# Optimization experiments

Hardware: AMD Instinct MI355X
Metric: run time of the kernel (lower is better)

The kernel has to match this reference:

```python
import jax, jax.numpy as jnp
import numpy as np

N_NODES = 2048
N_FLUID = 400000
N_SOLID = 400000


def setup_inputs() -> dict:
    key = jax.random.key(0)
    k1, k2, k3 = jax.random.split(key, 3)
    nodes = jax.random.uniform(k1, (N_NODES, 3), dtype=jnp.float32)
    # sorted distinct node ids per tet: sort 4 draws from [0, N-4) then add offsets 0..3
    fe = jnp.sort(jax.random.randint(k2, (N_FLUID, 4), 0, N_NODES - 4), axis=1) + jnp.arange(4)
    se = jnp.sort(jax.random.randint(k3, (N_SOLID, 4), 0, N_NODES - 4), axis=1) + jnp.arange(4)
    return {
        "nodes": nodes,
        "fluid_elements": fe.astype(jnp.int32),
        "solid_elements": se.astype(jnp.int32),
        "E_mod": jnp.float32(2.1e11),
        "nu": jnp.float32(0.3),
        "rho_s": jnp.float32(7850.0),
    }


def _grads_and_volume(coords):
    """coords: [E,4,3] -> shape-fn gradients [E,4,3], volume [E]."""
    ones = jnp.ones(coords.shape[:-1] + (1,), coords.dtype)
    A = jnp.concatenate([ones, coords], axis=-1)
    A_inv = jnp.linalg.inv(A)
    grads = jnp.swapaxes(A_inv[..., 1:, :], -1, -2)        # [E,4,3]
    v0 = coords[:, 1] - coords[:, 0]
    v1 = coords[:, 2] - coords[:, 0]
    v2 = coords[:, 3] - coords[:, 0]
    vol = jnp.abs(jnp.linalg.det(jnp.stack([v0, v1, v2], axis=-1))) / 6.0  # [E]
    return grads, vol


def _fluid_element_matrices(coords):
    grads, vol = _grads_and_volume(coords)
    K_e = vol[:, None, None] * jnp.einsum("eik,ejk->eij", grads, grads)      # [E,4,4]
    m_template = (2.0 * jnp.eye(4, dtype=coords.dtype) + jnp.ones((4, 4), coords.dtype)) / 10.0
    M_e = vol[:, None, None] * m_template
    return K_e, M_e


def _elasticity_D(E_mod, nu):
    coeff = E_mod / ((1.0 + nu) * (1.0 - 2.0 * nu))
    top = nu * jnp.ones((3, 3), jnp.float32) + (1.0 - 2.0 * nu) * jnp.eye(3, dtype=jnp.float32)
    D = jnp.zeros((6, 6), jnp.float32)
    D = D.at[:3, :3].set(top)
    D = D.at[3:, 3:].set(((1.0 - 2.0 * nu) / 2.0) * jnp.eye(3, dtype=jnp.float32))
    return coeff * D


def _solid_element_matrices(coords, E_mod, nu, rho_s):
    grads, vol = _grads_and_volume(coords)                 # grads [E,4,3]
    bx, by, bz = grads[..., 0], grads[..., 1], grads[..., 2]   # each [E,4]
    z = jnp.zeros_like(bx)
    # per-node 6x3 strain-displacement block -> [E,4,6,3]
    block = jnp.stack([
        jnp.stack([bx, z, z], axis=-1),
        jnp.stack([z, by, z], axis=-1),
        jnp.stack([z, z, bz], axis=-1),
        jnp.stack([by, bx, z], axis=-1),
        jnp.stack([z, bz, by], axis=-1),
        jnp.stack([bz, z, bx], axis=-1),
    ], axis=-2)
    E = coords.shape[0]
    B = jnp.transpose(block, (0, 2, 1, 3)).reshape(E, 6, 12)  # [E,6,12]
    D = _elasticity_D(E_mod, nu)                              # [6,6]
    K_e = vol[:, None, None] * jnp.einsum("eai,ab,ebj->eij", B, D, B)  # [E,12,12]
    M_e = (rho_s * vol / 4.0)[:, None, None] * jnp.eye(12, dtype=coords.dtype)
    return K_e, M_e


def reference(nodes, fluid_elements, solid_elements, E_mod, nu, rho_s):
    n = nodes.shape[0]
    # ---- fluid: local matrices + scatter-add assembly into [N,N] ----
    cf = nodes[fluid_elements]                              # [Ef,4,3]
    Kf_e, Mf_e = _fluid_element_matrices(cf)
    rows = fluid_elements[:, :, None]                       # [Ef,4,1]
    cols = fluid_elements[:, None, :]                       # [Ef,1,4]
    K_f = jnp.zeros((n, n), jnp.float32).at[rows, cols].add(Kf_e)
    M_f = jnp.zeros((n, n), jnp.float32).at[rows, cols].add(Mf_e)
    # ---- solid: 3 dof/node, assembly into [3N,3N] ----
    cs = nodes[solid_elements]                              # [Es,4,3]
    Ks_e, Ms_e = _solid_element_matrices(cs, E_mod, nu, rho_s)
    dofs = (3 * solid_elements[:, :, None] + jnp.arange(3)).reshape(solid_elements.shape[0], 12)
    K_s = jnp.zeros((3 * n, 3 * n), jnp.float32).at[dofs[:, :, None], dofs[:, None, :]].add(Ks_e)
    M_s = jnp.zeros((3 * n, 3 * n), jnp.float32).at[dofs[:, :, None], dofs[:, None, :]].add(Ms_e)
    return (K_f, M_f, K_s, M_s)
```

## Files before the change

### kernel.cpp

```cpp
#include <hip/hip_runtime.h>


#define G_PART 256
#define BT 512
#define GW (BT / 64)
#define TCAP 1024
#define NCPT 4
#define VSTRIDE 13

__device__ __forceinline__ float sel4(float x0, float x1, float x2, float x3, int a) {
    float r = x0;
    r = (a == 1) ? x1 : r;
    r = (a == 2) ? x2 : r;
    r = (a == 3) ? x3 : r;
    return r;
}
__device__ __forceinline__ int sel4i(int x0, int x1, int x2, int x3, int a) {
    int r = x0;
    r = (a == 1) ? x1 : r;
    r = (a == 2) ? x2 : r;
    r = (a == 3) ? x3 : r;
    return r;
}

__device__ __forceinline__ float wave_reduce(float v) {
#pragma unroll
    for (int m = 1; m < 64; m <<= 1) v += __shfl_xor(v, m, 64);
    return v;
}

__device__ __forceinline__ void tet_geom_f(const float* __restrict__ nodes,
                                           int n0, int n1, int n2, int n3_,
                                           float& gx1, float& gy1, float& gz1,
                                           float& gx2, float& gy2, float& gz2,
                                           float& gx3, float& gy3, float& gz3,
                                           float& volf)
{
    const float* q0 = nodes + 3ll * n0;
    const float* q1 = nodes + 3ll * n1;
    const float* q2 = nodes + 3ll * n2;
    const float* q3 = nodes + 3ll * n3_;
    double p0x = q0[0], p0y = q0[1], p0z = q0[2];
    double r1x = (double)q1[0] - p0x, r1y = (double)q1[1] - p0y, r1z = (double)q1[2] - p0z;
    double r2x = (double)q2[0] - p0x, r2y = (double)q2[1] - p0y, r2z = (double)q2[2] - p0z;
    double r3x = (double)q3[0] - p0x, r3y = (double)q3[1] - p0y, r3z = (double)q3[2] - p0z;
    double c23x = r2y*r3z - r2z*r3y, c23y = r2z*r3x - r2x*r3z, c23z = r2x*r3y - r2y*r3x;
    double det = r1x*c23x + r1y*c23y + r1z*c23z;
    double inv = 1.0 / det;
    double c31x = r3y*r1z - r3z*r1y, c31y = r3z*r1x - r3x*r1z, c31z = r3x*r1y - r3y*r1x;
    double c12x = r1y*r2z - r1z*r2y, c12y = r1z*r2x - r1x*r2z, c12z = r1x*r2y - r1y*r2x;
    gx1 = (float)(c23x*inv); gy1 = (float)(c23y*inv); gz1 = (float)(c23z*inv);
    gx2 = (float)(c31x*inv); gy2 = (float)(c31y*inv); gz2 = (float)(c31z*inv);
    gx3 = (float)(c12x*inv); gy3 = (float)(c12y*inv); gz3 = (float)(c12z*inv);
    volf = (float)(fabs(det) / 6.0);
}

__device__ __forceinline__ int fetch_entry_bs(const int* __restrict__ ent,
                                              const int* __restrict__ Sb,
                                              const int* __restrict__ Qb,
                                              int chunk4, int v)
{
    int lo = 0, hi = 255;
#pragma unroll
    for (int it = 0; it < 8; ++it) {
        int mid = (lo + hi + 1) >> 1;
        bool ge = (Qb[mid] <= v);
        lo = ge ? mid : lo;
        hi = ge ? hi : mid - 1;
    }
    return ent[(size_t)lo * chunk4 + Sb[lo] + (v - Qb[lo])];
}

__global__ void __launch_bounds__(256)
index_build(const int4* __restrict__ fe, const int4* __restrict__ se,
            int* __restrict__ entF, int* __restrict__ entS,
            int* __restrict__ PF, int* __restrict__ PS,
            int nf, int ns, int n, int chunkF, int chunkS)
{
    extern __shared__ int h[];
    int* wsum = h + n;
    const bool solid = blockIdx.x >= G_PART;
    const int b = solid ? blockIdx.x - G_PART : blockIdx.x;
    const int4* elems = solid ? se : fe;
    const int nelem = solid ? ns : nf;
    const int chunk = solid ? chunkS : chunkF;
    int* P2 = solid ? PS : PF;
    int* entries = (solid ? entS : entF) + (size_t)b * 4 * chunk;

    const int t = threadIdx.x;
    const int beg = b * chunk, end = min(nelem, beg + chunk);

    for (int i = t; i < n; i += 256) h[i] = 0;
    __syncthreads();
    for (int e = beg + t; e < end; e += 256) {
        int4 nd = elems[e];
        atomicAdd(&h[nd.x], 1);
        atomicAdd(&h[nd.y], 1);
        atomicAdd(&h[nd.z], 1);
        atomicAdd(&h[nd.w], 1);
    }
    __syncthreads();

    const int cs = (n + 255) / 256;
    const int base = t * cs;
    int s = 0;
    for (int k = 0; k < cs; ++k) {
        int i = base + k;
        if (i < n) s += h[i];
    }
    wsum[t] = s;
    __syncthreads();
    for (int d = 1; d < 256; d <<= 1) {
        int v = (t >= d) ? wsum[t - d] : 0;
        __syncthreads();
        wsum[t] += v;
        __syncthreads();
    }
    int run = (t == 0) ? 0 : wsum[t - 1];
    for (int k = 0; k < cs; ++k) {
        int i = base + k;
        if (i < n) {
            int c = h[i]; h[i] = run;
            P2[(size_t)i * G_PART + b] = run;
            run += c;
        }
    }
    if (t == 255) P2[(size_t)n * G_PART + b] = wsum[255];
    __syncthreads();

    for (int e = beg + t; e < end; e += 256) {
        int4 nd = elems[e];
        int p;
        p = atomicAdd(&h[nd.x], 1); entries[p] = e * 4 + 0;
        p = atomicAdd(&h[nd.y], 1); entries[p] = e * 4 + 1;
        p = atomicAdd(&h[nd.z], 1); entries[p] = e * 4 + 2;
        p = atomicAdd(&h[nd.w], 1); entries[p] = e * 4 + 3;
    }
}

__global__ void __launch_bounds__(BT, 2)
fused_gather(const int* __restrict__ entF, const int* __restrict__ PF,
             const int* __restrict__ entS, const int* __restrict__ PS,
             const int4* __restrict__ fe, const int4* __restrict__ se,
             const float* __restrict__ nodes,
             float* __restrict__ Kf, float* __restrict__ Mf,
             float* __restrict__ Ks, float* __restrict__ Ms,
             const float* __restrict__ E_p, const float* __restrict__ nu_p,
             const float* __restrict__ rho_p, int n, int n3,
             int chunk4F, int chunk4S)
{
    extern __shared__ unsigned char smem[];
    float* vis  = (float*)smem;
    int*   pcnt = (int*)(vis + TCAP * VSTRIDE);
    int*   plist = pcnt + n;
    int*   Sb   = plist + 3 * TCAP;
    int*   Qb   = Sb + 256;
    int*   wsp  = Qb + 257;
    float* dred = (float*)(wsp + GW);

    const int tid = threadIdx.x;
    const int bid = blockIdx.x;
    const bool isSolid = bid < n;
    const int r = isSolid ? bid : bid - n;
    const int* ent = isSolid ? entS : entF;
    const int* P2  = isSolid ? PS : PF;
    const int4* elems4 = isSolid ? se : fe;
    const int chunk4 = isSolid ? chunk4S : chunk4F;

    if (tid < 256) {
        int s0 = P2[(size_t)r * G_PART + tid];
        int e0 = P2[(size_t)(r + 1) * G_PART + tid];
        Sb[tid] = s0;
        Qb[tid] = e0 - s0;
    }
    __syncthreads();
    if (tid < 64) {
        int c0 = Qb[4*tid], c1 = Qb[4*tid+1], c2 = Qb[4*tid+2], c3 = Qb[4*tid+3];
        int s = c0 + c1 + c2 + c3;
        int x = s;
#pragma unroll
        for (int d = 1; d < 64; d <<= 1) {
            int y = __shfl_up(x, d, 64);
            if (tid >= d) x += y;
        }
        int ex = x - s;
        Qb[4*tid] = ex; Qb[4*tid+1] = ex + c0;
        Qb[4*tid+2] = ex + c0 + c1; Qb[4*tid+3] = ex + c0 + c1 + c2;
        if (tid == 63) Qb[256] = ex + s;
    }
    __syncthreads();
    const int T = Qb[256];

    const float E = *E_p, nu = *nu_p, rho = *rho_p;
    const float coeff = E / ((1.f + nu) * (1.f - 2.f * nu));
    const float lam = coeff * nu;
    const float mu  = coeff * (1.f - 2.f * nu) * 0.5f;

    if (isSolid) {
        float acc[NCPT][9];
#pragma unroll
        for (int k = 0; k < NCPT; ++k)
#pragma unroll
            for (int j = 0; j < 9; ++j) acc[k][j] = 0.f;
        float d00=0,d01=0,d02=0,d10=0,d11=0,d12=0,d20=0,d21=0,d22=0,vsum=0;

        for (int vb = 0; vb < T; vb += TCAP) {
            const int Tb = min(T - vb, TCAP);
            for (int c = tid; c < n; c += BT) pcnt[c] = 0;
            __syncthreads();

            for (int v = tid; v < Tb; v += BT) {
                int pk = fetch_entry_bs(ent, Sb, Qb, chunk4, vb + v);
                int e_ = pk >> 2, a = pk & 3;
                int4 nd = elems4[e_];
                float g1x,g1y,g1z,g2x,g2y,g2z,g3x,g3y,g3z,vol;
                tet_geom_f(nodes, nd.x, nd.y, nd.z, nd.w,
                           g1x,g1y,g1z, g2x,g2y,g2z, g3x,g3y,g3z, vol);
                float g0x = -(g1x+g2x+g3x), g0y = -(g1y+g2y+g3y), g0z = -(g1z+g2z+g3z);
                float* V = vis + v * VSTRIDE;
                V[0]=g1x; V[1]=g1y; V[2]=g1z; V[3]=g2x; V[4]=g2y; V[5]=g2z;
                V[6]=g3x; V[7]=g3y; V[8]=g3z; V[9]=vol;
                ((int*)V)[10] = nd.x | (nd.y << 11) | (a << 22);
                ((int*)V)[11] = nd.z | (nd.w << 11);
                float ga0 = sel4(g0x,g1x,g2x,g3x,a);
                float ga1 = sel4(g0y,g1y,g2y,g3y,a);
                float ga2 = sel4(g0z,g1z,g2z,g3z,a);
                {
                    float lv = lam*vol, mv = mu*vol, lm = lv+mv;
                    float mgg = mv*(ga0*ga0 + ga1*ga1 + ga2*ga2);
                    d00 += lm*ga0*ga0 + mgg; d01 += lm*ga0*ga1;       d02 += lm*ga0*ga2;
                    d10 += lm*ga1*ga0;       d11 += lm*ga1*ga1 + mgg; d12 += lm*ga1*ga2;
                    d20 += lm*ga2*ga0;       d21 += lm*ga2*ga1;       d22 += lm*ga2*ga2 + mgg;
                    vsum += vol;
                }
#pragma unroll
                for (int s = 0; s < 3; ++s) {
                    int b = s + ((s >= a) ? 1 : 0);
                    int cb = sel4i(nd.x, nd.y, nd.z, nd.w, b);
                    atomicAdd(&pcnt[cb], 1);
                }
            }
            __syncthreads();

            {
                const int cs = (n + BT - 1) / BT;
                int cb0 = tid * cs;
                int s = 0;
                for (int k = 0; k < cs; ++k) {
                    int i = cb0 + k;
                    if (i < n) s += pcnt[i];
                }
                int x = s;
#pragma unroll
                for (int d = 1; d < 64; d <<= 1) {
                    int y = __shfl_up(x, d, 64);
                    if ((tid & 63) >= d) x += y;
                }
                if ((tid & 63) == 63) wsp[tid >> 6] = x;
                __syncthreads();
                if (tid == 0) {
                    int run = 0;
                    for (int w = 0; w < GW; ++w) { int t_ = wsp[w]; wsp[w] = run; run += t_; }
                }
                __syncthreads();
                int ex = (x - s) + wsp[tid >> 6];
                for (int k = 0; k < cs; ++k) {
                    int i = cb0 + k;
                    if (i < n) { int c0 = pcnt[i]; pcnt[i] = ex; ex += c0; }
                }
            }
            __syncthreads();

            for (int v = tid; v < Tb; v += BT) {
                const float* V = vis + v * VSTRIDE;
                int w0 = ((const int*)V)[10], w1 = ((const int*)V)[11];
                int a = (w0 >> 22) & 3;
                int c0 = w0 & 2047, c1 = (w0 >> 11) & 2047;
                int c2 = w1 & 2047, c3 = (w1 >> 11) & 2047;
#pragma unroll
                for (int s = 0; s < 3; ++s) {
                    int b = s + ((s >= a) ? 1 : 0);
                    int cb = sel4i(c0, c1, c2, c3, b);
                    int p = atomicAdd(&pcnt[cb], 1);
                    plist[p] = (v << 4) | (a << 2) | b;
                }
            }
            __syncthreads();

#pragma unroll
            for (int k = 0; k < NCPT; ++k) {
                int c = tid + k * BT;
                if (c < n) {
                    int s0 = (c == 0) ? 0 : pcnt[c - 1];
                    int s1 = pcnt[c];
                    for (int p = s0; p < s1; ++p) {
                        int pe = plist[p];
                        int v = pe >> 4, a = (pe >> 2) & 3, b = pe & 3;
                        const float* V = vis + v * VSTRIDE;
                        float g1x=V[0],g1y=V[1],g1z=V[2],g2x=V[3],g2y=V[4],g2z=V[5],
                              g3x=V[6],g3y=V[7],g3z=V[8],vol=V[9];
                        float g0x=-(g1x+g2x+g3x), g0y=-(g1y+g2y+g3y), g0z=-(g1z+g2z+g3z);
                        float ga0=sel4(g0x,g1x,g2x,g3x,a);
                        float ga1=sel4(g0y,g1y,g2y,g3y,a);
                        float ga2=sel4(g0z,g1z,g2z,g3z,a);
                        float gb0=sel4(g0x,g1x,g2x,g3x,b);
                        float gb1=sel4(g0y,g1y,g2y,g3y,b);
                        float gb2=sel4(g0z,g1z,g2z,g3z,b);
                        float lv=lam*vol, mv=mu*vol;
                        float la0=lv*ga0, la1=lv*ga1, la2=lv*ga2;
                        float ma0=mv*ga0, ma1=mv*ga1, ma2=mv*ga2;
                        float mgg=mv*(ga0*gb0 + ga1*gb1 + ga2*gb2);
                        acc[k][0] += la0*gb0 + ma0*gb0 + mgg;
                        acc[k][1] += la0*gb1 + ma1*gb0;
                        acc[k][2] += la0*gb2 + ma2*gb0;
                        acc[k][3] += la1*gb0 + ma0*gb1;
                        acc[k][4] += la1*gb1 + ma1*gb1 + mgg;
                        acc[k][5] += la1*gb2 + ma2*gb1;
                        acc[k][6] += la2*gb0 + ma0*gb2;
                        acc[k][7] += la2*gb1 + ma1*gb2;
                        acc[k][8] += la2*gb2 + ma2*gb2 + mgg;
                    }
                }
            }
            __syncthreads();
        }

        d00=wave_reduce(d00); d01=wave_reduce(d01); d02=wave_reduce(d02);
        d10=wave_reduce(d10); d11=wave_reduce(d11); d12=wave_reduce(d12);
        d20=wave_reduce(d20); d21=wave_reduce(d21); d22=wave_reduce(d22);
        vsum=wave_reduce(vsum);
        if ((tid & 63) == 0) {
            int w = tid >> 6;
            dred[w*10+0]=d00; dred[w*10+1]=d01; dred[w*10+2]=d02;
            dred[w*10+3]=d10; dred[w*10+4]=d11; dred[w*10+5]=d12;
            dred[w*10+6]=d20; dred[w*10+7]=d21; dred[w*10+8]=d22;
            dred[w*10+9]=vsum;
        }
        __syncthreads();
        if (tid < 10) {
            float t_ = 0.f;
            for (int w = 0; w < GW; ++w) t_ += dred[w*10 + tid];
            dred[GW*10 + tid] = t_;
        }
        __syncthreads();

        const float msdiag = rho * 0.25f * dred[GW*10 + 9];
#pragma unroll
        for (int k = 0; k < NCPT; ++k) {
            int c = tid + k * BT;
            if (c < n) {
                bool dg = (c == r);
                float t0 = acc[k][0] + (dg ? dred[GW*10+0] : 0.f);
                float t1 = acc[k][1] + (dg ? dred[GW*10+1] : 0.f);
                float t2 = acc[k][2] + (dg ? dred[GW*10+2] : 0.f);
                float t3 = acc[k][3] + (dg ? dred[GW*10+3] : 0.f);
                float t4 = acc[k][4] + (dg ? dred[GW*10+4] : 0.f);
                float t5 = acc[k][5] + (dg ? dred[GW*10+5] : 0.f);
                float t6 = acc[k][6] + (dg ? dred[GW*10+6] : 0.f);
                float t7 = acc[k][7] + (dg ? dred[GW*10+7] : 0.f);
                float t8 = acc[k][8] + (dg ? dred[GW*10+8] : 0.f);
                size_t ro0 = (size_t)(3*r + 0) * n3 + 3*c;
                size_t ro1 = (size_t)(3*r + 1) * n3 + 3*c;
                size_t ro2 = (size_t)(3*r + 2) * n3 + 3*c;
                Ks[ro0+0]=t0; Ks[ro0+1]=t1; Ks[ro0+2]=t2;
                Ks[ro1+0]=t3; Ks[ro1+1]=t4; Ks[ro1+2]=t5;
                Ks[ro2+0]=t6; Ks[ro2+1]=t7; Ks[ro2+2]=t8;
                Ms[ro0+0] = dg ? msdiag : 0.f; Ms[ro0+1] = 0.f; Ms[ro0+2] = 0.f;
                Ms[ro1+0] = 0.f; Ms[ro1+1] = dg ? msdiag : 0.f; Ms[ro1+2] = 0.f;
                Ms[ro2+0] = 0.f; Ms[ro2+1] = 0.f; Ms[ro2+2] = dg ? msdiag : 0.f;
            }
        }
    } else {
        float accK[NCPT], accM[NCPT];
#pragma unroll
        for (int k = 0; k < NCPT; ++k) { accK[k] = 0.f; accM[k] = 0.f; }
        float dK = 0.f, dM = 0.f;

        for (int vb = 0; vb < T; vb += TCAP) {
            const int Tb = min(T - vb, TCAP);
            for (int c = tid; c < n; c += BT) pcnt[c] = 0;
            __syncthreads();

            for (int v = tid; v < Tb; v += BT) {
                int pk = fetch_entry_bs(ent, Sb, Qb, chunk4, vb + v);
                int e_ = pk >> 2, a = pk & 3;
                int4 nd = elems4[e_];
                float g1x,g1y,g1z,g2x,g2y,g2z,g3x,g3y,g3z,vol;
                tet_geom_f(nodes, nd.x, nd.y, nd.z, nd.w,
                           g1x,g1y,g1z, g2x,g2y,g2z, g3x,g3y,g3z, vol);
                float g0x = -(g1x+g2x+g3x), g0y = -(g1y+g2y+g3y), g0z = -(g1z+g2z+g3z);
                float* V = vis + v * VSTRIDE;
                V[0]=g1x; V[1]=g1y; V[2]=g1z; V[3]=g2x; V[4]=g2y; V[5]=g2z;
                V[6]=g3x; V[7]=g3y; V[8]=g3z; V[9]=vol;
                ((int*)V)[10] = nd.x | (nd.y << 11) | (a << 22);
                ((int*)V)[11] = nd.z | (nd.w << 11);
                float ga0 = sel4(g0x,g1x,g2x,g3x,a);
                float ga1 = sel4(g0y,g1y,g2y,g3y,a);
                float ga2 = sel4(g0z,g1z,g2z,g3z,a);
                dK += vol*(ga0*ga0 + ga1*ga1 + ga2*ga2);
                dM += vol*0.3f;
#pragma unroll
                for (int s = 0; s < 3; ++s) {
                    int b = s + ((s >= a) ? 1 : 0);
                    int cb = sel4i(nd.x, nd.y, nd.z, nd.w, b);
                    atomicAdd(&pcnt[cb], 1);
                }
            }
            __syncthreads();

            {
                const int cs = (n + BT - 1) / BT;
                int cb0 = tid * cs;
                int s = 0;
                for (int k = 0; k < cs; ++k) {
                    int i = cb0 + k;
                    if (i < n) s += pcnt[i];
                }
                int x = s;
#pragma unroll
                for (int d = 1; d < 64; d <<= 1) {
                    int y = __shfl_up(x, d, 64);
                    if ((tid & 63) >= d) x += y;
                }
                if ((tid & 63) == 63) wsp[tid >> 6] = x;
                __syncthreads();
                if (tid == 0) {
                    int run = 0;
                    for (int w = 0; w < GW; ++w) { int t_ = wsp[w]; wsp[w] = run; run += t_; }
                }
                __syncthreads();
                int ex = (x - s) + wsp[tid >> 6];
                for (int k = 0; k < cs; ++k) {
                    int i = cb0 + k;
                    if (i < n) { int c0 = pcnt[i]; pcnt[i] = ex; ex += c0; }
                }
            }
            __syncthreads();

            for (int v = tid; v < Tb; v += BT) {
                const float* V = vis + v * VSTRIDE;
                int w0 = ((const int*)V)[10], w1 = ((const int*)V)[11];
                int a = (w0 >> 22) & 3;
                int c0 = w0 & 2047, c1 = (w0 >> 11) & 2047;
                int c2 = w1 & 2047, c3 = (w1 >> 11) & 2047;
#pragma unroll
                for (int s = 0; s < 3; ++s) {
                    int b = s + ((s >= a) ? 1 : 0);
                    int cb = sel4i(c0, c1, c2, c3, b);
                    int p = atomicAdd(&pcnt[cb], 1);
                    plist[p] = (v << 4) | (a << 2) | b;
                }
            }
            __syncthreads();

#pragma unroll
            for (int k = 0; k < NCPT; ++k) {
                int c = tid + k * BT;
                if (c < n) {
                    int s0 = (c == 0) ? 0 : pcnt[c - 1];
                    int s1 = pcnt[c];
                    for (int p = s0; p < s1; ++p) {
                        int pe = plist[p];
                        int v = pe >> 4, a = (pe >> 2) & 3, b = pe & 3;
                        const float* V = vis + v * VSTRIDE;
                        float g1x=V[0],g1y=V[1],g1z=V[2],g2x=V[3],g2y=V[4],g2z=V[5],
                              g3x=V[6],g3y=V[7],g3z=V[8],vol=V[9];
                        float g0x=-(g1x+g2x+g3x), g0y=-(g1y+g2y+g3y), g0z=-(g1z+g2z+g3z);
                        float ga0=sel4(g0x,g1x,g2x,g3x,a);
                        float ga1=sel4(g0y,g1y,g2y,g3y,a);
                        float ga2=sel4(g0z,g1z,g2z,g3z,a);
                        float gb0=sel4(g0x,g1x,g2x,g3x,b);
                        float gb1=sel4(g0y,g1y,g2y,g3y,b);
                        float gb2=sel4(g0z,g1z,g2z,g3z,b);
                        accK[k] += vol*(ga0*gb0 + ga1*gb1 + ga2*gb2);
                        accM[k] += vol*0.1f;
                    }
                }
            }
            __syncthreads();
        }

        dK = wave_reduce(dK);
        dM = wave_reduce(dM);
        if ((tid & 63) == 0) { int w = tid >> 6; dred[w*2+0] = dK; dred[w*2+1] = dM; }
        __syncthreads();
        if (tid < 2) {
            float t_ = 0.f;
            for (int w = 0; w < GW; ++w) t_ += dred[w*2 + tid];
            dred[GW*2 + tid] = t_;
        }
        __syncthreads();

#pragma unroll
        for (int k = 0; k < NCPT; ++k) {
            int c = tid + k * BT;
            if (c < n) {
                bool dg = (c == r);
                Kf[(size_t)r * n + c] = accK[k] + (dg ? dred[GW*2+0] : 0.f);
                Mf[(size_t)r * n + c] = accM[k] + (dg ? dred[GW*2+1] : 0.f);
            }
        }
    }
}

__device__ __forceinline__ void tet_grads_d(const float* __restrict__ nodes,
                                            const int* ni, double g[4][3], double& vol)
{
    double p[4][3];
#pragma unroll
    for (int a = 0; a < 4; ++a) {
        const float* q = nodes + 3ll * ni[a];
        p[a][0] = (double)q[0]; p[a][1] = (double)q[1]; p[a][2] = (double)q[2];
    }
    double r1[3], r2[3], r3[3];
#pragma unroll
    for (int k = 0; k < 3; ++k) {
        r1[k] = p[1][k] - p[0][k];
        r2[k] = p[2][k] - p[0][k];
        r3[k] = p[3][k] - p[0][k];
    }
    double c23[3] = { r2[1]*r3[2]-r2[2]*r3[1], r2[2]*r3[0]-r2[0]*r3[2], r2[0]*r3[1]-r2[1]*r3[0] };
    double det = r1[0]*c23[0] + r1[1]*c23[1] + r1[2]*c23[2];
    double inv = 1.0 / det;
    double c31[3] = { r3[1]*r1[2]-r3[2]*r1[1], r3[2]*r1[0]-r3[0]*r1[2], r3[0]*r1[1]-r3[1]*r1[0] };
    double c12[3] = { r1[1]*r2[2]-r1[2]*r2[1], r1[2]*r2[0]-r1[0]*r2[2], r1[0]*r2[1]-r1[1]*r2[0] };
#pragma unroll
    for (int k = 0; k < 3; ++k) {
        g[1][k] = c23[k]*inv; g[2][k] = c31[k]*inv; g[3][k] = c12[k]*inv;
        g[0][k] = -(g[1][k] + g[2][k] + g[3][k]);
    }
    vol = fabs(det) / 6.0;
}

__global__ void __launch_bounds__(256)
fluid_assemble(const float* __restrict__ nodes, const int* __restrict__ elems,
               float* __restrict__ Kf, float* __restrict__ Mf, int nelem, int n)
{
    int e = blockIdx.x * blockDim.x + threadIdx.x;
    if (e >= nelem) return;
    const int4 nd = *reinterpret_cast<const int4*>(elems + 4ll * e);
    int ni[4] = { nd.x, nd.y, nd.z, nd.w };
    double g[4][3], vol;
    tet_grads_d(nodes, ni, g, vol);
#pragma unroll
    for (int a = 0; a < 4; ++a) {
        long long rowoff = (long long)ni[a] * n;
#pragma unroll
        for (int b = 0; b < 4; ++b) {
            double kv = vol * (g[a][0]*g[b][0] + g[a][1]*g[b][1] + g[a][2]*g[b][2]);
            double mv = vol * (a == b ? 0.3 : 0.1);
            atomicAdd(Kf + rowoff + ni[b], (float)kv);
            atomicAdd(Mf + rowoff + ni[b], (float)mv);
        }
    }
}

__global__ void __launch_bounds__(256)
solid_assemble(const float* __restrict__ nodes, const int* __restrict__ elems,
               float* __restrict__ Ks, float* __restrict__ Ms,
               const float* __restrict__ E_p, const float* __restrict__ nu_p,
               const float* __restrict__ rho_p, int nelem, int n3)
{
    int e = blockIdx.x * blockDim.x + threadIdx.x;
    if (e >= nelem) return;
    double E = (double)*E_p, nu = (double)*nu_p, rho = (double)*rho_p;
    double coeff = E / ((1.0 + nu) * (1.0 - 2.0 * nu));
    double lam = coeff * nu, mu = coeff * (1.0 - 2.0 * nu) * 0.5;
    const int4 nd = *reinterpret_cast<const int4*>(elems + 4ll * e);
    int ni[4] = { nd.x, nd.y, nd.z, nd.w };
    double g[4][3], vol;
    tet_grads_d(nodes, ni, g, vol);
    double lv = lam * vol, mv = mu * vol;
#pragma unroll
    for (int a = 0; a < 4; ++a) {
        long long row0 = 3ll * ni[a];
#pragma unroll
        for (int b = 0; b < 4; ++b) {
            long long col0 = 3ll * ni[b];
            double gg = g[a][0]*g[b][0] + g[a][1]*g[b][1] + g[a][2]*g[b][2];
#pragma unroll
            for (int i = 0; i < 3; ++i) {
                float* rowp = Ks + (row0 + i) * (long long)n3 + col0;
#pragma unroll
                for (int j = 0; j < 3; ++j) {
                    double val = lv * g[a][i] * g[b][j] + mv * g[a][j] * g[b][i];
                    if (i == j) val += mv * gg;
                    atomicAdd(rowp + j, (float)val);
                }
            }
        }
        float mval = (float)(rho * vol * 0.25);
#pragma unroll
        for (int i = 0; i < 3; ++i) {
            long long d = row0 + i;
            atomicAdd(Ms + d * (long long)n3 + d, mval);
        }
    }
}

extern "C" void kernel_launch(void* const* d_in, const int* in_sizes, int n_in,
                              void* d_out, int out_size, void* d_ws, size_t ws_size,
                              hipStream_t stream)
{
    const float* nodes = (const float*)d_in[0];
    const int*   fe    = (const int*)d_in[1];
    const int*   se    = (const int*)d_in[2];
    const float* E_p   = (const float*)d_in[3];
    const float* nu_p  = (const float*)d_in[4];
    const float* rho_p = (const float*)d_in[5];

    const int n  = in_sizes[0] / 3;
    const int nf = in_sizes[1] / 4;
    const int ns = in_sizes[2] / 4;
    const int n3 = 3 * n;

    float* out = (float*)d_out;
    float* Kf = out;
    float* Mf = Kf + (size_t)n * n;
    float* Ks = Mf + (size_t)n * n;
    float* Ms = Ks + (size_t)n3 * n3;

    const int chunkF = (nf + G_PART - 1) / G_PART;
    const int chunkS = (ns + G_PART - 1) / G_PART;

    size_t pos = 0;
    auto take = [&](size_t bytes) {
        size_t p = pos;
        pos = (pos + bytes + 255) & ~(size_t)255;
        return p;
    };
    size_t entF_o = take((size_t)4 * chunkF * G_PART * 4);
    size_t entS_o = take((size_t)4 * chunkS * G_PART * 4);
    size_t PF_o   = take((size_t)(n + 1) * G_PART * 4);
    size_t PS_o   = take((size_t)(n + 1) * G_PART * 4);

    size_t gatherLds = (size_t)TCAP * VSTRIDE * 4 + (size_t)n * 4
                     + (size_t)3 * TCAP * 4 + (256 + 257 + GW) * 4
                     + (GW * 10 + 10) * 4;
    size_t indexLds  = (size_t)(n + 256) * 4;
    bool gather_ok = (pos <= ws_size) && (n <= 2048) && (n <= NCPT * BT) &&
                     (gatherLds <= 80 * 1024) && (indexLds <= 64 * 1024);

    const int bs = 256;

    if (!gather_ok) {
        hipMemsetAsync(d_out, 0, (size_t)out_size * sizeof(float), stream);
        fluid_assemble<<<(nf + bs - 1) / bs, bs, 0, stream>>>(nodes, fe, Kf, Mf, nf, n);
        solid_assemble<<<(ns + bs - 1) / bs, bs, 0, stream>>>(nodes, se, Ks, Ms,
                                                              E_p, nu_p, rho_p, ns, n3);
        return;
    }

    char* ws = (char*)d_ws;
    int* entF = (int*)(ws + entF_o);
    int* entS = (int*)(ws + entS_o);
    int* PF   = (int*)(ws + PF_o);
    int* PS   = (int*)(ws + PS_o);

    const int4* fe4 = (const int4*)fe;
    const int4* se4 = (const int4*)se;

    index_build<<<2 * G_PART, bs, indexLds, stream>>>(fe4, se4, entF, entS, PF, PS,
                                                      nf, ns, n, chunkF, chunkS);
    fused_gather<<<2 * n, BT, gatherLds, stream>>>(entF, PF, entS, PS,
                                                   fe4, se4, nodes,
                                                   Kf, Mf, Ks, Ms,
                                                   E_p, nu_p, rho_p, n, n3,
                                                   4 * chunkF, 4 * chunkS);
}
```

Before: 184.5 us.

## Stage entry lists in LDS, unroll staging two-wide, and vectorize solid row writes

When a row's entry count fits in one tile, the block copies its entry list into shared memory once, so later reads skip the per-entry binary-search fetch. The staging loop now handles exactly two entries per thread, so both element index loads are issued before either geometry computation. The solid K rows are first built in shared memory and then written as coalesced float4 stores, and M rows are written directly as float4. This adds extra barriers and narrows the fast path to n divisible by 4 with a size check on the shared buffer.

```diff
diff --git a/kernel.cpp b/kernel.cpp
--- a/kernel.cpp
+++ b/kernel.cpp
@@ -190,6 +190,15 @@
     }
     __syncthreads();
     const int T = Qb[256];
+    const bool fast = (T <= TCAP);
+    int* entLds = plist;
+
+    if (fast && tid < 256) {
+        int q0 = Qb[tid], q1 = Qb[tid + 1];
+        const int* src = ent + (size_t)tid * chunk4 + Sb[tid];
+        for (int k = 0; k < q1 - q0; ++k) entLds[q0 + k] = src[k];
+    }
+    __syncthreads();
 
     const float E = *E_p, nu = *nu_p, rho = *rho_p;
     const float coeff = E / ((1.f + nu) * (1.f - 2.f * nu));
@@ -204,41 +213,50 @@
             for (int j = 0; j < 9; ++j) acc[k][j] = 0.f;
         float d00=0,d01=0,d02=0,d10=0,d11=0,d12=0,d20=0,d21=0,d22=0,vsum=0;
 
+#define STAGE_S(v_, a_, nd_) do { \
+            float g1x,g1y,g1z,g2x,g2y,g2z,g3x,g3y,g3z,vol; \
+            tet_geom_f(nodes, (nd_).x, (nd_).y, (nd_).z, (nd_).w, \
+                       g1x,g1y,g1z, g2x,g2y,g2z, g3x,g3y,g3z, vol); \
+            float g0x = -(g1x+g2x+g3x), g0y = -(g1y+g2y+g3y), g0z = -(g1z+g2z+g3z); \
+            float* V = vis + (v_) * VSTRIDE; \
+            V[0]=g1x; V[1]=g1y; V[2]=g1z; V[3]=g2x; V[4]=g2y; V[5]=g2z; \
+            V[6]=g3x; V[7]=g3y; V[8]=g3z; V[9]=vol; \
+            ((int*)V)[10] = (nd_).x | ((nd_).y << 11) | ((a_) << 22); \
+            ((int*)V)[11] = (nd_).z | ((nd_).w << 11); \
+            float ga0 = sel4(g0x,g1x,g2x,g3x,(a_)); \
+            float ga1 = sel4(g0y,g1y,g2y,g3y,(a_)); \
+            float ga2 = sel4(g0z,g1z,g2z,g3z,(a_)); \
+            { \
+                float lv = lam*vol, mv = mu*vol, lm = lv+mv; \
+                float mgg = mv*(ga0*ga0 + ga1*ga1 + ga2*ga2); \
+                d00 += lm*ga0*ga0 + mgg; d01 += lm*ga0*ga1;       d02 += lm*ga0*ga2; \
+                d10 += lm*ga1*ga0;       d11 += lm*ga1*ga1 + mgg; d12 += lm*ga1*ga2; \
+                d20 += lm*ga2*ga0;       d21 += lm*ga2*ga1;       d22 += lm*ga2*ga2 + mgg; \
+                vsum += vol; \
+            } \
+            _Pragma("unroll") \
+            for (int s_ = 0; s_ < 3; ++s_) { \
+                int b_ = s_ + ((s_ >= (a_)) ? 1 : 0); \
+                int cb_ = sel4i((nd_).x, (nd_).y, (nd_).z, (nd_).w, b_); \
+                atomicAdd(&pcnt[cb_], 1); \
+            } \
+        } while (0)
+
         for (int vb = 0; vb < T; vb += TCAP) {
             const int Tb = min(T - vb, TCAP);
             for (int c = tid; c < n; c += BT) pcnt[c] = 0;
             __syncthreads();
 
-            for (int v = tid; v < Tb; v += BT) {
-                int pk = fetch_entry_bs(ent, Sb, Qb, chunk4, vb + v);
-                int e_ = pk >> 2, a = pk & 3;
-                int4 nd = elems4[e_];
-                float g1x,g1y,g1z,g2x,g2y,g2z,g3x,g3y,g3z,vol;
-                tet_geom_f(nodes, nd.x, nd.y, nd.z, nd.w,
-                           g1x,g1y,g1z, g2x,g2y,g2z, g3x,g3y,g3z, vol);
-                float g0x = -(g1x+g2x+g3x), g0y = -(g1y+g2y+g3y), g0z = -(g1z+g2z+g3z);
-                float* V = vis + v * VSTRIDE;
-                V[0]=g1x; V[1]=g1y; V[2]=g1z; V[3]=g2x; V[4]=g2y; V[5]=g2z;
-                V[6]=g3x; V[7]=g3y; V[8]=g3z; V[9]=vol;
-                ((int*)V)[10] = nd.x | (nd.y << 11) | (a << 22);
-                ((int*)V)[11] = nd.z | (nd.w << 11);
-                float ga0 = sel4(g0x,g1x,g2x,g3x,a);
-                float ga1 = sel4(g0y,g1y,g2y,g3y,a);
-                float ga2 = sel4(g0z,g1z,g2z,g3z,a);
-                {
-                    float lv = lam*vol, mv = mu*vol, lm = lv+mv;
-                    float mgg = mv*(ga0*ga0 + ga1*ga1 + ga2*ga2);
-                    d00 += lm*ga0*ga0 + mgg; d01 += lm*ga0*ga1;       d02 += lm*ga0*ga2;
-                    d10 += lm*ga1*ga0;       d11 += lm*ga1*ga1 + mgg; d12 += lm*ga1*ga2;
-                    d20 += lm*ga2*ga0;       d21 += lm*ga2*ga1;       d22 += lm*ga2*ga2 + mgg;
-                    vsum += vol;
-                }
-#pragma unroll
-                for (int s = 0; s < 3; ++s) {
-                    int b = s + ((s >= a) ? 1 : 0);
-                    int cb = sel4i(nd.x, nd.y, nd.z, nd.w, b);
-                    atomicAdd(&pcnt[cb], 1);
-                }
+            {
+                int v0 = tid, v1 = tid + BT;
+                int pk0 = -1, pk1 = -1;
+                if (v0 < Tb) pk0 = fast ? entLds[v0] : fetch_entry_bs(ent, Sb, Qb, chunk4, vb + v0);
+                if (v1 < Tb) pk1 = fast ? entLds[v1] : fetch_entry_bs(ent, Sb, Qb, chunk4, vb + v1);
+                int4 nd0 = make_int4(0,0,0,0), nd1 = make_int4(0,0,0,0);
+                if (pk0 >= 0) nd0 = elems4[pk0 >> 2];
+                if (pk1 >= 0) nd1 = elems4[pk1 >> 2];
+                if (pk0 >= 0) { int a0 = pk0 & 3; STAGE_S(v0, a0, nd0); }
+                if (pk1 >= 0) { int a1 = pk1 & 3; STAGE_S(v1, a1, nd1); }
             }
             __syncthreads();
 
@@ -344,67 +362,82 @@
         }
         __syncthreads();
 
+        float* plane = (float*)vis;
+        const int q = n3 >> 2;
+#pragma unroll
+        for (int i = 0; i < 3; ++i) {
+#pragma unroll
+            for (int k = 0; k < NCPT; ++k) {
+                int c = tid + k * BT;
+                if (c < n) {
+                    bool dg = (c == r);
+                    plane[3*c+0] = acc[k][i*3+0] + (dg ? dred[GW*10 + i*3+0] : 0.f);
+                    plane[3*c+1] = acc[k][i*3+1] + (dg ? dred[GW*10 + i*3+1] : 0.f);
+                    plane[3*c+2] = acc[k][i*3+2] + (dg ? dred[GW*10 + i*3+2] : 0.f);
+                }
+            }
+            __syncthreads();
+            float4* dst = (float4*)(Ks + (size_t)(3*r + i) * n3);
+            for (int t4 = tid; t4 < q; t4 += BT) dst[t4] = ((const float4*)plane)[t4];
+            __syncthreads();
+        }
         const float msdiag = rho * 0.25f * dred[GW*10 + 9];
-#pragma unroll
-        for (int k = 0; k < NCPT; ++k) {
-            int c = tid + k * BT;
-            if (c < n) {
-                bool dg = (c == r);
-                float t0 = acc[k][0] + (dg ? dred[GW*10+0] : 0.f);
-                float t1 = acc[k][1] + (dg ? dred[GW*10+1] : 0.f);
-                float t2 = acc[k][2] + (dg ? dred[GW*10+2] : 0.f);
-                float t3 = acc[k][3] + (dg ? dred[GW*10+3] : 0.f);
-                float t4 = acc[k][4] + (dg ? dred[GW*10+4] : 0.f);
-                float t5 = acc[k][5] + (dg ? dred[GW*10+5] : 0.f);
-                float t6 = acc[k][6] + (dg ? dred[GW*10+6] : 0.f);
-                float t7 = acc[k][7] + (dg ? dred[GW*10+7] : 0.f);
-                float t8 = acc[k][8] + (dg ? dred[GW*10+8] : 0.f);
-                size_t ro0 = (size_t)(3*r + 0) * n3 + 3*c;
-                size_t ro1 = (size_t)(3*r + 1) * n3 + 3*c;
-                size_t ro2 = (size_t)(3*r + 2) * n3 + 3*c;
-                Ks[ro0+0]=t0; Ks[ro0+1]=t1; Ks[ro0+2]=t2;
-                Ks[ro1+0]=t3; Ks[ro1+1]=t4; Ks[ro1+2]=t5;
-                Ks[ro2+0]=t6; Ks[ro2+1]=t7; Ks[ro2+2]=t8;
-                Ms[ro0+0] = dg ? msdiag : 0.f; Ms[ro0+1] = 0.f; Ms[ro0+2] = 0.f;
-                Ms[ro1+0] = 0.f; Ms[ro1+1] = dg ? msdiag : 0.f; Ms[ro1+2] = 0.f;
-                Ms[ro2+0] = 0.f; Ms[ro2+1] = 0.f; Ms[ro2+2] = dg ? msdiag : 0.f;
-            }
+        for (int k4 = tid; k4 < 3 * q; k4 += BT) {
+            int i = (k4 >= q) + (k4 >= 2*q);
+            int t4 = k4 - i * q;
+            int dcol = 3*r + i;
+            int base = t4 << 2;
+            float4 w;
+            w.x = (base + 0 == dcol) ? msdiag : 0.f;
+            w.y = (base + 1 == dcol) ? msdiag : 0.f;
+            w.z = (base + 2 == dcol) ? msdiag : 0.f;
+            w.w = (base + 3 == dcol) ? msdiag : 0.f;
+            ((float4*)(Ms + (size_t)(3*r + i) * n3))[t4] = w;
         }
     } else {
         float accK[NCPT], accM[NCPT];
 #pragma unroll
         for (int k = 0; k < NCPT; ++k) { accK[k] = 0.f; accM[k] = 0.f; }
         float dK = 0.f, dM = 0.f;
+
+#define STAGE_F(v_, a_, nd_) do { \
+            float g1x,g1y,g1z,g2x,g2y,g2z,g3x,g3y,g3z,vol; \
+            tet_geom_f(nodes, (nd_).x, (nd_).y, (nd_).z, (nd_).w, \
+                       g1x,g1y,g1z, g2x,g2y,g2z, g3x,g3y,g3z, vol); \
+            float g0x = -(g1x+g2x+g3x), g0y = -(g1y+g2y+g3y), g0z = -(g1z+g2z+g3z); \
+            float* V = vis + (v_) * VSTRIDE; \
+            V[0]=g1x; V[1]=g1y; V[2]=g1z; V[3]=g2x; V[4]=g2y; V[5]=g2z; \
+            V[6]=g3x; V[7]=g3y; V[8]=g3z; V[9]=vol; \
+            ((int*)V)[10] = (nd_).x | ((nd_).y << 11) | ((a_) << 22); \
+            ((int*)V)[11] = (nd_).z | ((nd_).w << 11); \
+            float ga0 = sel4(g0x,g1x,g2x,g3x,(a_)); \
+            float ga1 = sel4(g0y,g1y,g2y,g3y,(a_)); \
+            float ga2 = sel4(g0z,g1z,g2z,g3z,(a_)); \
+            dK += vol*(ga0*ga0 + ga1*ga1 + ga2*ga2); \
+            dM += vol*0.3f; \
+            _Pragma("unroll") \
+            for (int s_ = 0; s_ < 3; ++s_) { \
+                int b_ = s_ + ((s_ >= (a_)) ? 1 : 0); \
+                int cb_ = sel4i((nd_).x, (nd_).y, (nd_).z, (nd_).w, b_); \
+                atomicAdd(&pcnt[cb_], 1); \
+            } \
+        } while (0)
 
         for (int vb = 0; vb < T; vb += TCAP) {
             const int Tb = min(T - vb, TCAP);
             for (int c = tid; c < n; c += BT) pcnt[c] = 0;
             __syncthreads();
 
-            for (int v = tid; v < Tb; v += BT) {
-                int pk = fetch_entry_bs(ent, Sb, Qb, chunk4, vb + v);
-                int e_ = pk >> 2, a = pk & 3;
-                int4 nd = elems4[e_];
-                float g1x,g1y,g1z,g2x,g2y,g2z,g3x,g3y,g3z,vol;
-                tet_geom_f(nodes, nd.x, nd.y, nd.z, nd.w,
-                           g1x,g1y,g1z, g2x,g2y,g2z, g3x,g3y,g3z, vol);
-                float g0x = -(g1x+g2x+g3x), g0y = -(g1y+g2y+g3y), g0z = -(g1z+g2z+g3z);
-                float* V = vis + v * VSTRIDE;
-                V[0]=g1x; V[1]=g1y; V[2]=g1z; V[3]=g2x; V[4]=g2y; V[5]=g2z;
-                V[6]=g3x; V[7]=g3y; V[8]=g3z; V[9]=vol;
-                ((int*)V)[10] = nd.x | (nd.y << 11) | (a << 22);
-                ((int*)V)[11] = nd.z | (nd.w << 11);
-                float ga0 = sel4(g0x,g1x,g2x,g3x,a);
-                float ga1 = sel4(g0y,g1y,g2y,g3y,a);
-                float ga2 = sel4(g0z,g1z,g2z,g3z,a);
-                dK += vol*(ga0*ga0 + ga1*ga1 + ga2*ga2);
-                dM += vol*0.3f;
-#pragma unroll
-                for (int s = 0; s < 3; ++s) {
-                    int b = s + ((s >= a) ? 1 : 0);
-                    int cb = sel4i(nd.x, nd.y, nd.z, nd.w, b);
-                    atomicAdd(&pcnt[cb], 1);
-                }
+            {
+                int v0 = tid, v1 = tid + BT;
+                int pk0 = -1, pk1 = -1;
+                if (v0 < Tb) pk0 = fast ? entLds[v0] : fetch_entry_bs(ent, Sb, Qb, chunk4, vb + v0);
+                if (v1 < Tb) pk1 = fast ? entLds[v1] : fetch_entry_bs(ent, Sb, Qb, chunk4, vb + v1);
+                int4 nd0 = make_int4(0,0,0,0), nd1 = make_int4(0,0,0,0);
+                if (pk0 >= 0) nd0 = elems4[pk0 >> 2];
+                if (pk1 >= 0) nd1 = elems4[pk1 >> 2];
+                if (pk0 >= 0) { int a0 = pk0 & 3; STAGE_F(v0, a0, nd0); }
+                if (pk1 >= 0) { int a1 = pk1 & 3; STAGE_F(v1, a1, nd1); }
             }
             __syncthreads();
 
@@ -638,7 +671,8 @@
                      + (size_t)3 * TCAP * 4 + (256 + 257 + GW) * 4
                      + (GW * 10 + 10) * 4;
     size_t indexLds  = (size_t)(n + 256) * 4;
-    bool gather_ok = (pos <= ws_size) && (n <= 2048) && (n <= NCPT * BT) &&
+    bool gather_ok = (pos <= ws_size) && (n <= 2048) && ((n & 3) == 0) &&
+                     (n <= NCPT * BT) && (3 * n <= TCAP * VSTRIDE) &&
                      (gatherLds <= 80 * 1024) && (indexLds <= 64 * 1024);
 
     const int bs = 256;
```

Result: slower. 191.8 us (+4.0%).
